# Kernel optimization log

Measured on AMD Instinct MI355X. Metric: run time of the kernel, lower is better.

## Reference

```python
import jax, jax.numpy as jnp
import numpy as np

TEMPERATURE = 0.05
BETA = 1.0
LAMBDA_THRESHOLD = 0.7


def setup_inputs() -> dict:
    key = jax.random.key(0)
    k1, k2 = jax.random.split(key)
    B, D = 8192, 256
    features = jax.random.normal(k1, (B, D), dtype=jnp.float32)
    labels = jax.random.randint(k2, (B,), 0, 100, dtype=jnp.int64)
    return {"features": features, "labels": labels}


def reference(features, labels):
    B = features.shape[0]
    eps = 1e-12
    # L2 normalize rows
    f = features / jnp.maximum(jnp.linalg.norm(features, axis=1, keepdims=True), eps)
    sim = jnp.matmul(f, f.T) / TEMPERATURE                      # [B, B]
    sim_max = jnp.max(sim, axis=1, keepdims=True)               # [B, 1]
    sim_stable = sim - sim_max

    same = (labels[:, None] == labels[None, :])
    eye = jnp.eye(B, dtype=bool)
    pos_mask = same & ~eye                                       # [B, B] bool

    # Denominator: logsumexp over all non-self entries per row
    exp_sim = jnp.exp(sim_stable) * (~eye)
    log_denom = jnp.log(jnp.sum(exp_sim, axis=1, keepdims=True) + eps) + sim_max  # [B,1]

    # SCL term: mean over positive pairs of (log_denom[i] - sim[i,j])
    pos_f = pos_mask.astype(sim.dtype)
    n_pos = jnp.sum(pos_f)
    scl_sum = jnp.sum(pos_f * (log_denom - sim))
    scl_loss = jnp.where(n_pos > 0, scl_sum / jnp.maximum(n_pos, 1.0), 0.0)

    # Relaxation term: per row, logsumexp over high-sim positive logits + baseline
    high = (sim * TEMPERATURE > LAMBDA_THRESHOLD) & pos_mask     # [B, B] bool
    neg_inf = jnp.asarray(-jnp.inf, sim.dtype)
    masked_logits = jnp.where(high, sim_stable, neg_inf)          # [B, B]
    baseline = (1.0 / TEMPERATURE) - sim_max                      # [B, 1]
    all_logits = jnp.concatenate([masked_logits, baseline], axis=1)  # [B, B+1]
    row_lse = jax.nn.logsumexp(all_logits, axis=1)                # [B]
    row_has = jnp.any(high, axis=1)
    n_high = jnp.sum(high.astype(sim.dtype))
    relax_sum = jnp.sum(jnp.where(row_has, row_lse, 0.0))
    relaxation_loss = jnp.where(n_high > 0, relax_sum / jnp.maximum(n_high, 1.0), 0.0)

    total = scl_loss + BETA * relaxation_loss
    return jnp.clip(total, 0.0, 10.0)
```

## Files before the change

### kernel.cpp

```cpp
#include <hip/hip_runtime.h>
#include <hip/hip_bf16.h>
#include <math.h>

#define B_N 8192
#define D_K 256
#define TILE 128
#define NT 256
#define NBLK 64
#define NPAIR 2080
#define NCLS 100
#define KEXP 28.8539008177792681f
#define KCH 32
#define NCHUNK 8
#define APAD 2048

typedef __attribute__((ext_vector_type(8))) short short8;
typedef __attribute__((ext_vector_type(4))) float f32x4;

template <bool V> struct BoolC { static constexpr bool value = V; };

__device__ __forceinline__ unsigned short f2bf(float x) {
    unsigned int u = __float_as_uint(x);
    unsigned int r = (u + 0x7FFFu + ((u >> 16) & 1u)) >> 16;
    return (unsigned short)r;
}

__device__ __forceinline__ void gload_lds16(const short* g, short* l) {
    __builtin_amdgcn_global_load_lds(
        (const __attribute__((address_space(1))) void*)g,
        (__attribute__((address_space(3))) void*)l, 16, 0, 0);
}

__device__ __forceinline__ float row_sum16(float v) {
    v += __int_as_float(__builtin_amdgcn_update_dpp(0, __float_as_int(v), 0xB1, 0xF, 0xF, true));
    v += __int_as_float(__builtin_amdgcn_update_dpp(0, __float_as_int(v), 0x4E, 0xF, 0xF, true));
    v += __int_as_float(__builtin_amdgcn_update_dpp(0, __float_as_int(v), 0x141, 0xF, 0xF, true));
    v += __int_as_float(__builtin_amdgcn_update_dpp(0, __float_as_int(v), 0x140, 0xF, 0xF, true));
    return v;
}

__global__ void prep_kernel(const float* __restrict__ feat, unsigned short* __restrict__ fnorm,
                            const int* __restrict__ labels, int* __restrict__ cnt,
                            float* __restrict__ gscal, double* __restrict__ accum,
                            unsigned int* __restrict__ done) {
    if (blockIdx.x == 0) {
        __shared__ int h[NCLS];
        int t = threadIdx.x;
        if (t < NCLS) h[t] = 0;
        if (t == 0) {
            gscal[0] = 0.f; gscal[1] = 0.f;
            accum[0] = 0.0; accum[1] = 0.0; accum[2] = 0.0;
            *done = 0u;
        }
        __syncthreads();
        for (int r = t; r < B_N; r += 256) atomicAdd(&h[labels[r]], 1);
        __syncthreads();
        if (t < NCLS) cnt[t] = h[t];
    }
    int wave = threadIdx.x >> 6, lane = threadIdx.x & 63;
    int row = blockIdx.x * 4 + wave;
    float4 v = *(const float4*)(feat + (size_t)row * D_K + lane * 4);
    float ss = v.x * v.x + v.y * v.y + v.z * v.z + v.w * v.w;
    #pragma unroll
    for (int off = 1; off < 64; off <<= 1) ss += __shfl_xor(ss, off);
    float inv = 1.0f / fmaxf(sqrtf(ss), 1e-12f);
    ushort4 o;
    o.x = f2bf(v.x * inv); o.y = f2bf(v.y * inv);
    o.z = f2bf(v.z * inv); o.w = f2bf(v.w * inv);
    *(ushort4*)(fnorm + (size_t)row * D_K + lane * 4) = o;
}

__global__ __launch_bounds__(NT, 3) void main_kernel(
        const unsigned short* __restrict__ fnorm, const int* __restrict__ labels,
        float2* __restrict__ G, float* __restrict__ gscal) {
    int bid = blockIdx.x;
    int b = (int)((sqrtf(8.0f * bid + 1.0f) - 1.0f) * 0.5f);
    while ((b + 1) * (b + 2) / 2 <= bid) ++b;
    while (b * (b + 1) / 2 > bid) --b;
    int a = bid - b * (b + 1) / 2;
    const int row0 = a * TILE, col0 = b * TILE;
    const bool diag = (a == b);

    __shared__ short As[2][TILE * KCH + APAD];
    __shared__ short Bs[2][TILE * KCH];
    __shared__ int Ls[2 * TILE];
    __shared__ float2 Rbuf[2 * TILE];
    __shared__ float2 Cbuf[2 * TILE];
    __shared__ int ghs[4];
    __shared__ float gps[4];

    const int tid = threadIdx.x;
    const int lane = tid & 63, wave = tid >> 6;
    const int wm = wave >> 1, wn = wave & 1;
    const int l15 = lane & 15, lhi = lane >> 4;
    const short* fn = (const short*)fnorm;

    const int rbase = (tid >> 2) * D_K + (((tid & 3) ^ ((tid >> 3) & 3))) * 8;
    const int uds = (tid & ~63) * 8;

    if (tid < 128) Ls[tid] = labels[row0 + tid];
    else Ls[tid] = labels[col0 + tid - 128];
    if (lane == 0) ghs[wave] = 0;

    const int abase = row0 * D_K + rbase;
    const int bbase = col0 * D_K + rbase;

    gload_lds16(fn + abase, &As[0][uds]);
    gload_lds16(fn + abase + 64 * D_K, &As[0][2048 + uds]);
    if (!diag) {
        gload_lds16(fn + bbase, &Bs[0][uds]);
        gload_lds16(fn + bbase + 64 * D_K, &Bs[0][2048 + uds]);
    }

    f32x4 acc[4][4];
    #pragma unroll
    for (int i = 0; i < 4; i++)
        #pragma unroll
        for (int j = 0; j < 4; j++) acc[i][j] = {0.f, 0.f, 0.f, 0.f};

    const int ch8 = (lhi ^ ((l15 >> 1) & 3)) * 8;
    int aoff[4], boff[4];
    #pragma unroll
    for (int i = 0; i < 4; i++) {
        aoff[i] = (wm * 64 + i * 16 + l15) * KCH + ch8;
        boff[i] = (wn * 64 + i * 16 + l15) * KCH + ch8;
    }

    #pragma unroll
    for (int kc = 0; kc < NCHUNK; ++kc) {
        const int cur = kc & 1;
        __syncthreads();
        if (kc < NCHUNK - 1) {
            const int nxt = cur ^ 1, ko = (kc + 1) * KCH;
            gload_lds16(fn + abase + ko, &As[nxt][uds]);
            gload_lds16(fn + abase + 64 * D_K + ko, &As[nxt][2048 + uds]);
            if (!diag) {
                gload_lds16(fn + bbase + ko, &Bs[nxt][uds]);
                gload_lds16(fn + bbase + 64 * D_K + ko, &Bs[nxt][2048 + uds]);
            }
        }
        const short* Asrc = As[cur];
        const short* Bsrc = diag ? As[cur] : Bs[cur];
        short8 af[4], bfr[4];
        #pragma unroll
        for (int mi = 0; mi < 4; mi++) af[mi] = *(const short8*)&Asrc[aoff[mi]];
        #pragma unroll
        for (int ni = 0; ni < 4; ni++) bfr[ni] = *(const short8*)&Bsrc[boff[ni]];
        #pragma unroll
        for (int mi = 0; mi < 4; mi++)
            #pragma unroll
            for (int ni = 0; ni < 4; ni++)
                acc[mi][ni] = __builtin_amdgcn_mfma_f32_16x16x32_bf16(af[mi], bfr[ni], acc[mi][ni], 0, 0, 0);
    }

    int lc[4], colg[4];
    #pragma unroll
    for (int ni = 0; ni < 4; ni++) {
        int c = wn * 64 + ni * 16 + l15;
        lc[ni] = Ls[128 + c];
        colg[ni] = col0 + c;
    }

    auto body = [&](auto DIAGC) {
        constexpr bool DIAG = decltype(DIAGC)::value;
        float cD[4] = {0.f, 0.f, 0.f, 0.f};
        float gp = 0.f;
        bool anyhi = false;

        #pragma unroll
        for (int mi = 0; mi < 4; mi++) {
            #pragma unroll
            for (int reg = 0; reg < 4; reg++) {
                int rloc = wm * 64 + mi * 16 + lhi * 4 + reg;
                int rowg = row0 + rloc;
                int lr = Ls[rloc];
                float d = 0.f;
                #pragma unroll
                for (int ni = 0; ni < 4; ni++) {
                    float dot = acc[mi][ni][reg];
                    float e = __builtin_exp2f((dot - 1.0f) * KEXP);
                    bool ns = !DIAG || (rowg != colg[ni]);
                    float ev = ns ? e : 0.f;
                    d += ev; cD[ni] += ev;
                    bool ps = ns && (lr == lc[ni]);
                    gp += ps ? dot : 0.f;
                    anyhi = anyhi | (ps & (dot > 0.7f));
                }
                d = row_sum16(d);
                if (l15 == 0) Rbuf[wn * 128 + rloc] = {d, 0.f};
            }
        }

        if (!DIAG) {
            #pragma unroll
            for (int ni = 0; ni < 4; ni++) {
                cD[ni] += __shfl_xor(cD[ni], 16);
                cD[ni] += __shfl_xor(cD[ni], 32);
            }
            if (lhi == 0) {
                #pragma unroll
                for (int ni = 0; ni < 4; ni++)
                    Cbuf[wm * 128 + wn * 64 + ni * 16 + l15] = {cD[ni], 0.f};
            }
        }

        gp = row_sum16(gp);
        gp += __shfl_xor(gp, 16);
        gp += __shfl_xor(gp, 32);
        if (lane == 0) gps[wave] = gp;

        if (__any(anyhi)) {
            float cR[4] = {0.f, 0.f, 0.f, 0.f};
            int nhi = 0;
            #pragma unroll
            for (int mi = 0; mi < 4; mi++) {
                #pragma unroll
                for (int reg = 0; reg < 4; reg++) {
                    int rloc = wm * 64 + mi * 16 + lhi * 4 + reg;
                    int rowg = row0 + rloc;
                    int lr = Ls[rloc];
                    float rx = 0.f;
                    #pragma unroll
                    for (int ni = 0; ni < 4; ni++) {
                        float dot = acc[mi][ni][reg];
                        bool ns = !DIAG || (rowg != colg[ni]);
                        bool hi = ns && (lr == lc[ni]) && (dot > 0.7f);
                        float e = hi ? __builtin_exp2f((dot - 1.0f) * KEXP) : 0.f;
                        rx += e; cR[ni] += e; nhi += hi ? 1 : 0;
                    }
                    rx = row_sum16(rx);
                    if (l15 == 0) Rbuf[wn * 128 + rloc].y = rx;
                }
            }
            if (!DIAG) {
                #pragma unroll
                for (int ni = 0; ni < 4; ni++) {
                    cR[ni] += __shfl_xor(cR[ni], 16);
                    cR[ni] += __shfl_xor(cR[ni], 32);
                }
                if (lhi == 0) {
                    #pragma unroll
                    for (int ni = 0; ni < 4; ni++)
                        Cbuf[wm * 128 + wn * 64 + ni * 16 + l15].y = cR[ni];
                }
            }
            #pragma unroll
            for (int off = 1; off < 64; off <<= 1) nhi += __shfl_xor(nhi, off);
            if (lane == 0) ghs[wave] = nhi;
        }
    };
    if (diag) body(BoolC<true>{});
    else body(BoolC<false>{});
    __syncthreads();

    if (tid < 128) {
        int r = tid;
        float2 a0 = Rbuf[r], a1 = Rbuf[128 + r];
        G[(size_t)b * B_N + row0 + r] = {a0.x + a1.x, a0.y + a1.y};
    } else if (!diag) {
        int c = tid - 128;
        float2 a0 = Cbuf[c], a1 = Cbuf[128 + c];
        G[(size_t)a * B_N + col0 + c] = {a0.x + a1.x, a0.y + a1.y};
    }
    if (tid == 0) {
        float w = diag ? 1.0f : 2.0f;
        float gpt = gps[0] + gps[1] + gps[2] + gps[3];
        atomicAdd(&gscal[0], w * gpt);
        int tot = ghs[0] + ghs[1] + ghs[2] + ghs[3];
        if (tot > 0) atomicAdd(&gscal[1], w * (float)tot);
    }
}

__global__ void finalize_kernel(const float2* __restrict__ G, const int* __restrict__ labels,
                                const int* __restrict__ cnt, const float* __restrict__ gscal,
                                double* __restrict__ accum, unsigned int* __restrict__ done,
                                float* __restrict__ out) {
    int lane = threadIdx.x & 63, q = threadIdx.x >> 6;
    int r = blockIdx.x * 64 + lane;
    float d = 0.f, rx = 0.f;
    #pragma unroll
    for (int s = 0; s < 16; ++s) {
        float2 g = G[(size_t)(q * 16 + s) * B_N + r];
        d += g.x; rx += g.y;
    }
    __shared__ float2 sh[4][64];
    sh[q][lane] = {d, rx};
    __syncthreads();
    if (threadIdx.x < 64) {
        int rr = blockIdx.x * 64 + threadIdx.x;
        float2 t0 = sh[0][threadIdx.x], t1 = sh[1][threadIdx.x];
        float2 t2 = sh[2][threadIdx.x], t3 = sh[3][threadIdx.x];
        float dd = t0.x + t1.x + t2.x + t3.x;
        float rr2 = t0.y + t1.y + t2.y + t3.y;
        float np = (float)(cnt[labels[rr]] - 1);
        float ld = logf(dd + 1e-12f) + 20.0f;
        double s1 = (double)np * (double)ld;
        double s2 = (double)np;
        double s3 = (rr2 > 0.f) ? (double)logf(rr2 + 1.0f) : 0.0;
        #pragma unroll
        for (int off = 1; off < 64; off <<= 1) {
            s1 += __shfl_xor(s1, off);
            s2 += __shfl_xor(s2, off);
            s3 += __shfl_xor(s3, off);
        }
        if (threadIdx.x == 0) {
            atomicAdd(&accum[0], s1);
            atomicAdd(&accum[1], s2);
            atomicAdd(&accum[2], s3);
            __threadfence();
            unsigned int tk = atomicAdd(done, 1u);
            if (tk == gridDim.x - 1) {
                double a1 = atomicAdd(&accum[0], 0.0);
                double a2 = atomicAdd(&accum[1], 0.0);
                double a3 = atomicAdd(&accum[2], 0.0);
                double gp = (double)gscal[0];
                double gh = (double)gscal[1];
                double scl = (a2 > 0.0) ? (a1 - 20.0 * gp) / fmax(a2, 1.0) : 0.0;
                double rel = (gh > 0.0) ? a3 / fmax(gh, 1.0) : 0.0;
                double tot = scl + rel;
                tot = fmin(fmax(tot, 0.0), 10.0);
                out[0] = (float)tot;
            }
        }
    }
}

extern "C" void kernel_launch(void* const* d_in, const int* in_sizes, int n_in,
                              void* d_out, int out_size, void* d_ws, size_t ws_size,
                              hipStream_t stream) {
    const float* feat = (const float*)d_in[0];
    const int* labels = (const int*)d_in[1];
    float* out = (float*)d_out;
    char* ws = (char*)d_ws;

    unsigned short* fnorm = (unsigned short*)(ws);
    float2* G          = (float2*)(ws + (size_t)4 * 1024 * 1024);
    int*    cnt        = (int*)(ws + (size_t)8 * 1024 * 1024);
    float*  gscal      = (float*)(ws + (size_t)8 * 1024 * 1024 + 1024);
    double* accum      = (double*)(ws + (size_t)8 * 1024 * 1024 + 2048);
    unsigned int* done = (unsigned int*)(ws + (size_t)8 * 1024 * 1024 + 3072);

    prep_kernel<<<B_N / 4, 256, 0, stream>>>(feat, fnorm, labels, cnt, gscal, accum, done);
    main_kernel<<<NPAIR, NT, 0, stream>>>(fnorm, labels, G, gscal);
    finalize_kernel<<<B_N / 64, 256, 0, stream>>>(G, labels, cnt, gscal, accum, done, out);
    (void)in_sizes; (void)n_in; (void)out_size; (void)ws_size;
}
```

Measured before the change: 130.4 us.

## Load GEMM operand fragments directly from global into registers, bypassing LDS

Drops the double-buffered LDS staging of the normalized bf16 features. Each wave now loads its own MFMA fragments straight from global memory into registers, with a one-step register prefetch of the next K slice. This removes the LDS traffic, the swizzled address setup and the per-chunk barriers, and it frees LDS, which may raise occupancy. In exchange, fragments shared between waves are reloaded from global/L2 instead of being reused from LDS, the 16-byte loads are strided by rows, and register pressure goes up.

```diff
diff --git a/kernel.cpp b/kernel.cpp
--- a/kernel.cpp
+++ b/kernel.cpp
@@ -10,9 +10,6 @@
 #define NPAIR 2080
 #define NCLS 100
 #define KEXP 28.8539008177792681f
-#define KCH 32
-#define NCHUNK 8
-#define APAD 2048
 
 typedef __attribute__((ext_vector_type(8))) short short8;
 typedef __attribute__((ext_vector_type(4))) float f32x4;
@@ -23,12 +20,6 @@
     unsigned int u = __float_as_uint(x);
     unsigned int r = (u + 0x7FFFu + ((u >> 16) & 1u)) >> 16;
     return (unsigned short)r;
-}
-
-__device__ __forceinline__ void gload_lds16(const short* g, short* l) {
-    __builtin_amdgcn_global_load_lds(
-        (const __attribute__((address_space(1))) void*)g,
-        (__attribute__((address_space(3))) void*)l, 16, 0, 0);
 }
 
 __device__ __forceinline__ float row_sum16(float v) {
@@ -81,8 +72,6 @@
     const int row0 = a * TILE, col0 = b * TILE;
     const bool diag = (a == b);
 
-    __shared__ short As[2][TILE * KCH + APAD];
-    __shared__ short Bs[2][TILE * KCH];
     __shared__ int Ls[2 * TILE];
     __shared__ float2 Rbuf[2 * TILE];
     __shared__ float2 Cbuf[2 * TILE];
@@ -95,22 +84,12 @@
     const int l15 = lane & 15, lhi = lane >> 4;
     const short* fn = (const short*)fnorm;
 
-    const int rbase = (tid >> 2) * D_K + (((tid & 3) ^ ((tid >> 3) & 3))) * 8;
-    const int uds = (tid & ~63) * 8;
-
     if (tid < 128) Ls[tid] = labels[row0 + tid];
     else Ls[tid] = labels[col0 + tid - 128];
     if (lane == 0) ghs[wave] = 0;
 
-    const int abase = row0 * D_K + rbase;
-    const int bbase = col0 * D_K + rbase;
-
-    gload_lds16(fn + abase, &As[0][uds]);
-    gload_lds16(fn + abase + 64 * D_K, &As[0][2048 + uds]);
-    if (!diag) {
-        gload_lds16(fn + bbase, &Bs[0][uds]);
-        gload_lds16(fn + bbase + 64 * D_K, &Bs[0][2048 + uds]);
-    }
+    const int arow = (row0 + wm * 64 + l15) * D_K + lhi * 8;
+    const int brow = (col0 + wn * 64 + l15) * D_K + lhi * 8;
 
     f32x4 acc[4][4];
     #pragma unroll
@@ -118,40 +97,34 @@
         #pragma unroll
         for (int j = 0; j < 4; j++) acc[i][j] = {0.f, 0.f, 0.f, 0.f};
 
-    const int ch8 = (lhi ^ ((l15 >> 1) & 3)) * 8;
-    int aoff[4], boff[4];
+    short8 a0[4], b0[4];
     #pragma unroll
     for (int i = 0; i < 4; i++) {
-        aoff[i] = (wm * 64 + i * 16 + l15) * KCH + ch8;
-        boff[i] = (wn * 64 + i * 16 + l15) * KCH + ch8;
-    }
-
-    #pragma unroll
-    for (int kc = 0; kc < NCHUNK; ++kc) {
-        const int cur = kc & 1;
-        __syncthreads();
-        if (kc < NCHUNK - 1) {
-            const int nxt = cur ^ 1, ko = (kc + 1) * KCH;
-            gload_lds16(fn + abase + ko, &As[nxt][uds]);
-            gload_lds16(fn + abase + 64 * D_K + ko, &As[nxt][2048 + uds]);
-            if (!diag) {
-                gload_lds16(fn + bbase + ko, &Bs[nxt][uds]);
-                gload_lds16(fn + bbase + 64 * D_K + ko, &Bs[nxt][2048 + uds]);
-            }
-        }
-        const short* Asrc = As[cur];
-        const short* Bsrc = diag ? As[cur] : Bs[cur];
-        short8 af[4], bfr[4];
-        #pragma unroll
-        for (int mi = 0; mi < 4; mi++) af[mi] = *(const short8*)&Asrc[aoff[mi]];
-        #pragma unroll
-        for (int ni = 0; ni < 4; ni++) bfr[ni] = *(const short8*)&Bsrc[boff[ni]];
+        a0[i] = *(const short8*)(fn + arow + i * 16 * D_K);
+        b0[i] = *(const short8*)(fn + brow + i * 16 * D_K);
+    }
+    #pragma unroll
+    for (int ks = 0; ks < 8; ++ks) {
+        short8 a1[4], b1[4];
+        if (ks < 7) {
+            const int ko = (ks + 1) * 32;
+            #pragma unroll
+            for (int i = 0; i < 4; i++) {
+                a1[i] = *(const short8*)(fn + arow + i * 16 * D_K + ko);
+                b1[i] = *(const short8*)(fn + brow + i * 16 * D_K + ko);
+            }
+        }
         #pragma unroll
         for (int mi = 0; mi < 4; mi++)
             #pragma unroll
             for (int ni = 0; ni < 4; ni++)
-                acc[mi][ni] = __builtin_amdgcn_mfma_f32_16x16x32_bf16(af[mi], bfr[ni], acc[mi][ni], 0, 0, 0);
-    }
+                acc[mi][ni] = __builtin_amdgcn_mfma_f32_16x16x32_bf16(a0[mi], b0[ni], acc[mi][ni], 0, 0, 0);
+        if (ks < 7) {
+            #pragma unroll
+            for (int i = 0; i < 4; i++) { a0[i] = a1[i]; b0[i] = b1[i]; }
+        }
+    }
+    __syncthreads();
 
     int lc[4], colg[4];
     #pragma unroll
@@ -255,12 +228,12 @@
 
     if (tid < 128) {
         int r = tid;
-        float2 a0 = Rbuf[r], a1 = Rbuf[128 + r];
-        G[(size_t)b * B_N + row0 + r] = {a0.x + a1.x, a0.y + a1.y};
+        float2 a0v = Rbuf[r], a1v = Rbuf[128 + r];
+        G[(size_t)b * B_N + row0 + r] = {a0v.x + a1v.x, a0v.y + a1v.y};
     } else if (!diag) {
         int c = tid - 128;
-        float2 a0 = Cbuf[c], a1 = Cbuf[128 + c];
-        G[(size_t)a * B_N + col0 + c] = {a0.x + a1.x, a0.y + a1.y};
+        float2 a0v = Cbuf[c], a1v = Cbuf[128 + c];
+        G[(size_t)a * B_N + col0 + c] = {a0v.x + a1v.x, a0v.y + a1v.y};
     }
     if (tid == 0) {
         float w = diag ? 1.0f : 2.0f;
```

New measurement: 168.3 us. 29.1% more time.
